# Performance work log

Hardware: AMD Instinct MI355X
Metric: run time of the kernel (lower is better)

Reference implementation:

```python
import jax, jax.numpy as jnp
import numpy as np

B, T, NCH, NBIN, NBAND = 2, 400, 8, 512, 40
NPV = NCH * NCH


def setup_inputs() -> dict:
    key = jax.random.key(0)
    ks = jax.random.split(key, 7)
    bins_real = jax.random.normal(ks[0], (B, T, NCH, NBIN), jnp.float32)
    bins_imag = jax.random.normal(ks[1], (B, T, NCH, NBIN), jnp.float32)
    band_matrix_real = jax.random.normal(ks[2], (NBIN, NBAND), jnp.float32) * 0.05
    band_matrix_imag = jax.random.normal(ks[3], (NBIN, NBAND), jnp.float32) * 0.05
    cov_to_pv_real = jax.random.normal(ks[4], (NPV, NCH * NCH), jnp.float32) * 0.1
    cov_to_pv_imag = jax.random.normal(ks[5], (NPV, NCH * NCH), jnp.float32) * 0.1
    tau = jax.random.uniform(ks[6], (NBAND,), jnp.float32, 0.8, 0.99)
    return {
        'bins_real': bins_real, 'bins_imag': bins_imag,
        'band_matrix_real': band_matrix_real, 'band_matrix_imag': band_matrix_imag,
        'cov_to_pv_real': cov_to_pv_real, 'cov_to_pv_imag': cov_to_pv_imag,
        'tau': tau,
    }


def _power_vector(bins_real, bins_imag, band_matrix_real, band_matrix_imag,
                  cov_to_pv_real, cov_to_pv_imag, tau):
    x = jax.lax.complex(bins_real, bins_imag)            # (B,T,C,F)
    nch = x.shape[-2]
    EPS = 1e-20
    # per-bin covariance outer product, flattened cov dim: (B,T,F,C*C)
    cov = jnp.einsum('btif,btjf->btfij', x, jnp.conj(x))
    b, t, f = cov.shape[:3]
    cov = cov.reshape(b, t, f, nch * nch)
    diag = jnp.arange(nch) * (nch + 1)                   # diagonal indices in cov dim
    trace = jnp.clip(jnp.sum(cov.real[..., diag], axis=-1, keepdims=True), EPS, None)
    cov = cov / trace                                    # per-bin trace normalisation
    # phase adjustment along the bin axis (n=1 -> lag of 2 bins)
    c = jnp.swapaxes(cov, -1, -2)                        # (B,T,C2,F)
    prod = jnp.conj(c[..., :-2]) * c[..., 2:]
    ang = jnp.arctan2(prod.imag, prod.real)
    ang = jnp.concatenate([ang[..., :1], ang, ang[..., -1:]], axis=-1)  # edge pad
    adj = jnp.abs(c) * jax.lax.complex(jnp.cos(ang), jnp.sin(ang))
    adj = adj.at[..., diag, :].set(c[..., diag, :])      # keep original diagonals
    # band projection: contract bins against (F,K) band matrix
    bm = jax.lax.complex(band_matrix_real, band_matrix_imag)
    band_cov = jnp.einsum('btcf,fk->btkc', adj, bm)      # (B,T,K,C2)
    dsum = jnp.clip(band_cov.real[..., diag].sum(-1, keepdims=True), EPS, None)
    band_cov = band_cov / dsum
    # first-order IIR smoothing over frames, per-band pole tau
    a = tau[:, None].astype(band_cov.real.dtype)         # (K,1)
    def step(carry, xt):
        y = a * carry + (1.0 - a) * xt
        return y, y
    y0 = jnp.zeros_like(band_cov[:, 0])                  # (B,K,C2)
    _, ys = jax.lax.scan(step, y0, jnp.moveaxis(band_cov, 1, 0))
    band_cov = jnp.moveaxis(ys, 0, 1)                    # (B,T,K,C2)
    # cov -> power vector projection, real part
    c2p = jax.lax.complex(cov_to_pv_real, cov_to_pv_imag)  # (P,C2)
    pv = jnp.einsum('pc,btkc->btkp', c2p, band_cov).real   # (B,T,K,P)
    return pv


def reference(bins_real, bins_imag, band_matrix_real, band_matrix_imag,
              cov_to_pv_real, cov_to_pv_imag, tau):
    return _power_vector(bins_real, bins_imag, band_matrix_real, band_matrix_imag,
                         cov_to_pv_real, cov_to_pv_imag, tau)
```

## Files before the change

kernel.cpp:

```cpp
#include <hip/hip_runtime.h>
#include <hip/hip_fp16.h>

#define B_    2
#define T_    400
#define NCH_  8
#define NBIN_ 512
#define NBAND_ 40
#define NPV_  64

using half8   = __attribute__((ext_vector_type(8))) _Float16;
using float4v = __attribute__((ext_vector_type(4))) float;

static __device__ inline unsigned pkhf(float x, float y) {
  __half2 h = __float22half2_rn(make_float2(x, y));
  return __builtin_bit_cast(unsigned, h);
}
static __device__ inline unsigned rot16(unsigned u) {
  return (u >> 16) | (u << 16);
}
static __device__ inline unsigned cmulc(unsigned viu, unsigned vju) {
  __half2 Vi = __builtin_bit_cast(__half2, viu);
  __half2 Vj = __builtin_bit_cast(__half2, vju);
  __half2 P1 = __hmul2(Vi, __low2half2(Vj));
  __half2 Qi = __lowhigh2highlow(Vi);
  unsigned tn = __builtin_bit_cast(unsigned, __high2half2(Vj)) ^ 0x80000000u;
  __half2 a  = __hfma2(Qi, __builtin_bit_cast(__half2, tn), P1);
  return __builtin_bit_cast(unsigned, a);
}

__global__ __launch_bounds__(256) void pv_prep(
    const float* __restrict__ bmr, const float* __restrict__ bmi,
    const float* __restrict__ c2pr, const float* __restrict__ c2pi,
    float* __restrict__ ws)
{
  const int tid = threadIdx.x;
  const int blk = blockIdx.x;
  if (blk == 0) {
    __shared__ float sds[256];
    int k = tid & 63, part = tid >> 6;
    float s = 0.f;
    if (k < NBAND_) {
      const float* col = bmr + k;
      #pragma unroll 16
      for (int f = part * 128; f < part * 128 + 128; f++) s += col[f * 40];
    }
    sds[tid] = s;
    __syncthreads();
    if (tid < NBAND_) {
      float t = sds[tid] + sds[tid + 64] + sds[tid + 128] + sds[tid + 192];
      ws[tid] = 1.0f / fmaxf(t, 1e-20f);
    }
  } else if (blk <= 24) {
    int F = (blk - 1) * 256 + tid;
    int l = F & 63;
    int fid = F >> 6;
    int s5 = fid / 3;
    int n = fid - s5 * 3;
    int k = n * 16 + (l & 15);
    int quad = l >> 4;
    unsigned dw[4];
    #pragma unroll
    for (int t2 = 0; t2 < 4; t2++) {
      float v0 = 0.f, v1 = 0.f;
      if (k < NBAND_) {
        int f = s5 * 16 + quad * 4 + t2;
        v0 = bmr[f * 40 + k]; v1 = bmi[f * 40 + k];
      }
      dw[t2] = pkhf(v0, v1);
    }
    ((uint4*)((char*)ws + 1024))[F] = make_uint4(dw[0], dw[1], dw[2], dw[3]);
  } else {
    int F2 = (blk - 25) * 256 + tid;
    int lane = F2 & 63, E = F2 >> 6;
    int nt = E >> 2, ks = E & 3;
    int n = lane & 15, quad = lane >> 4;
    int p = nt * 16 + n;
    unsigned dw[4];
    #pragma unroll
    for (int t2 = 0; t2 < 4; t2++) {
      int c = ks * 16 + quad * 4 + t2;
      dw[t2] = pkhf(c2pr[p * 64 + c], -c2pi[p * 64 + c]);
    }
    ((uint4*)((char*)ws + 197632))[E * 64 + lane] = make_uint4(dw[0], dw[1], dw[2], dw[3]);
  }
}

__global__ __launch_bounds__(256, 3) void pv_main(
    const float* __restrict__ br, const float* __restrict__ bi,
    const float* __restrict__ ws, float* __restrict__ out)
{
  __shared__ __align__(16) unsigned smem[12288];

  const int bt  = blockIdx.x;
  const int tid = threadIdx.x;

  const int mt   = tid >> 6;
  const int lane = tid & 63;
  const int m16  = lane & 15;
  const int quad = lane >> 4;
  const int p    = mt * 16 + m16;
  const int ich  = p >> 3, jch = p & 7;
  const uint4* BF0 = (const uint4*)((const char*)ws + 1024);
  unsigned* vsh = smem + 8192;

  {
    const float4* gr4 = (const float4*)(br + (size_t)bt * (NCH_ * NBIN_));
    const float4* gi4 = (const float4*)(bi + (size_t)bt * (NCH_ * NBIN_));
    float4* lr4 = (float4*)smem;
    float4* li4 = (float4*)(smem + 4096);
    #pragma unroll
    for (int it = 0; it < 4; it++) {
      lr4[it * 256 + tid] = gr4[it * 256 + tid];
      li4[it * 256 + tid] = gi4[it * 256 + tid];
    }
  }
  __syncthreads();

  {
    const float* rr = (const float*)smem;
    const float* ri = (const float*)(smem + 4096);
    #pragma unroll
    for (int fs = 0; fs < 2; fs++) {
      const int f = fs * 256 + tid;
      const int fm = (f == 0) ? 0 : ((f == 511) ? 509 : f - 1);
      const int fp = (f == 0) ? 2 : ((f == 511) ? 511 : f + 1);
      float tr = 0.f;
      float t1[8], t2[8];
      #pragma unroll
      for (int c = 0; c < 8; c++) {
        const float* cr = rr + c * 512;
        const float* ci = ri + c * 512;
        float xr = cr[f],   xi = ci[f];
        float xrm = cr[fm], xim = ci[fm];
        float xrp = cr[fp], xip = ci[fp];
        tr = fmaf(xr, xr, tr); tr = fmaf(xi, xi, tr);
        float Gr = fmaf(xrm, xrp,  xim * xip);
        float Gi = fmaf(xrm, xip, -(xim * xrp));
        float am = fmaxf(fmaxf(fabsf(Gr), fabsf(Gi)), 1e-30f);
        float rc = __builtin_amdgcn_rcpf(am);
        float q1 = Gr * rc, q2 = Gi * rc;
        float n2 = fmaf(q1, q1, q2 * q2);
        float rn = __builtin_amdgcn_rsqf(n2);
        bool ok = n2 > 0.f;
        float ur = ok ? q1 * rn : 1.f;
        float ui = ok ? q2 * rn : 0.f;
        float mg = __builtin_amdgcn_sqrtf(fmaf(xr, xr, xi * xi));
        t1[c] = mg * ur; t2[c] = mg * ui;
      }
      float scv = __builtin_amdgcn_rsqf(fmaxf(tr, 1e-20f));
      const int fc = f >> 2, fl = f & 3;
      #pragma unroll
      for (int c = 0; c < 8; c++)
        vsh[c * 512 + ((fc ^ c) << 2) + fl] = pkhf(t1[c] * scv, t2[c] * scv);
    }
  }
  __syncthreads();

  float4v acc[6];
  #pragma unroll
  for (int g = 0; g < 6; g++) acc[g] = (float4v){0.f, 0.f, 0.f, 0.f};

  const uint4* Bg = BF0 + lane;
  uint4 pa0 = Bg[0],   pa1 = Bg[64],  pa2 = Bg[128];
  uint4 pb0 = Bg[192], pb1 = Bg[256], pb2 = Bg[320];
  #pragma unroll 4
  for (int s = 0; s < 32; s++) {
    uint4 cb0 = pa0, cb1 = pa1, cb2 = pa2;
    pa0 = pb0; pa1 = pb1; pa2 = pb2;
    {
      const uint4* nx = Bg + (size_t)(((s + 2) & 31) * 192);
      pb0 = nx[0]; pb1 = nx[64]; pb2 = nx[128];
    }
    const int sc = s * 4 + quad;
    half8 b0 = __builtin_bit_cast(half8, cb0);
    half8 b1 = __builtin_bit_cast(half8, cb1);
    half8 b2 = __builtin_bit_cast(half8, cb2);
    const uint4* vb = (const uint4*)vsh;
    uint4 av = vb[ich * 128 + (sc ^ ich)];
    uint4 bv = vb[jch * 128 + (sc ^ jch)];
    unsigned a0 = cmulc(av.x, bv.x);
    unsigned a1 = cmulc(av.y, bv.y);
    unsigned a2 = cmulc(av.z, bv.z);
    unsigned a3 = cmulc(av.w, bv.w);
    uint4 au1 = make_uint4(a0 ^ 0x80000000u, a1 ^ 0x80000000u,
                           a2 ^ 0x80000000u, a3 ^ 0x80000000u);
    uint4 au2 = make_uint4(rot16(a0), rot16(a1),
                           rot16(a2), rot16(a3));
    half8 af1 = __builtin_bit_cast(half8, au1);
    half8 af2 = __builtin_bit_cast(half8, au2);
    acc[0] = __builtin_amdgcn_mfma_f32_16x16x32_f16(af1, b0, acc[0], 0, 0, 0);
    acc[3] = __builtin_amdgcn_mfma_f32_16x16x32_f16(af2, b0, acc[3], 0, 0, 0);
    acc[1] = __builtin_amdgcn_mfma_f32_16x16x32_f16(af1, b1, acc[1], 0, 0, 0);
    acc[4] = __builtin_amdgcn_mfma_f32_16x16x32_f16(af2, b1, acc[4], 0, 0, 0);
    acc[2] = __builtin_amdgcn_mfma_f32_16x16x32_f16(af1, b2, acc[2], 0, 0, 0);
    acc[5] = __builtin_amdgcn_mfma_f32_16x16x32_f16(af2, b2, acc[5], 0, 0, 0);
  }
  __syncthreads();

  const uint4* EF = ((const uint4*)((const char*)ws + 197632)) + (mt * 4) * 64 + lane;
  uint4 eb[4];
  #pragma unroll
  for (int ks = 0; ks < 4; ks++) eb[ks] = EF[ks * 64];

  {
    unsigned* bcsh = smem;
    #pragma unroll
    for (int n = 0; n < 3; n++) {
      uint4 w4 = make_uint4(pkhf(acc[n][0], acc[n+3][0]),
                            pkhf(acc[n][1], acc[n+3][1]),
                            pkhf(acc[n][2], acc[n+3][2]),
                            pkhf(acc[n][3], acc[n+3][3]));
      *(uint4*)(bcsh + (n * 16 + m16) * 68 + mt * 16 + quad * 4) = w4;
    }
  }
  __syncthreads();

  const float4* wsd = (const float4*)ws;
  {
    const unsigned* bcsh = smem;
    float4v eacc[3];
    #pragma unroll
    for (int kt = 0; kt < 3; kt++) eacc[kt] = (float4v){0.f, 0.f, 0.f, 0.f};
    #pragma unroll
    for (int ks = 0; ks < 4; ks++) {
      half8 bfr = __builtin_bit_cast(half8, eb[ks]);
      #pragma unroll
      for (int kt = 0; kt < 3; kt++) {
        uint4 a4 = *(const uint4*)(bcsh + (kt * 16 + m16) * 68 + ks * 16 + quad * 4);
        half8 afr = __builtin_bit_cast(half8, a4);
        eacc[kt] = __builtin_amdgcn_mfma_f32_16x16x32_f16(afr, bfr, eacc[kt], 0, 0, 0);
      }
    }
    float* op = out + (size_t)bt * (NBAND_ * NPV_);
    #pragma unroll
    for (int kt = 0; kt < 3; kt++) {
      float4 dv = wsd[kt * 4 + quad];
      float dva[4] = {dv.x, dv.y, dv.z, dv.w};
      #pragma unroll
      for (int r = 0; r < 4; r++) {
        int k = kt * 16 + quad * 4 + r;
        if (k < NBAND_)
          op[k * 64 + mt * 16 + m16] = eacc[kt][r] * dva[r];
      }
    }
  }
}

__global__ __launch_bounds__(512) void pv_iir4(float* __restrict__ z,
                                               const float* __restrict__ tau)
{
  __shared__ float gsh[16][32];
  const int ph = blockIdx.x & 1;
  const int bk = blockIdx.x >> 1;
  const int k = bk % NBAND_;
  const int b = bk / NBAND_;
  const float a  = tau[k];
  const float om = 1.0f - a;
  const int c  = threadIdx.x >> 5;
  const int pl = threadIdx.x & 31;
  const int p  = ph * 32 + pl;
  const size_t stride = (size_t)NBAND_ * 64;
  size_t idx0 = (size_t)b * (T_ * NBAND_ * 64) + (size_t)(c * 25) * stride + k * 64 + p;

  float y[25];
  float accv = 0.f;
  #pragma unroll
  for (int i = 0; i < 25; i++) {
    float v = z[idx0 + (size_t)i * stride];
    accv = fmaf(a, accv, om * v);
    y[i] = accv;
  }
  gsh[c][pl] = accv;
  __syncthreads();
  float a2 = a * a, a4 = a2 * a2, a8 = a4 * a4, a16 = a8 * a8;
  float A = a16 * a8 * a;
  float H = 0.f;
  #pragma unroll
  for (int d = 0; d < 15; d++) {
    float g = gsh[d][pl];
    H = (d < c) ? fmaf(A, H, g) : H;
  }
  float wp = a;
  #pragma unroll
  for (int i = 0; i < 25; i++) {
    z[idx0 + (size_t)i * stride] = fmaf(wp, H, y[i]);
    wp *= a;
  }
}

extern "C" void kernel_launch(void* const* d_in, const int* in_sizes, int n_in,
                              void* d_out, int out_size, void* d_ws, size_t ws_size,
                              hipStream_t stream)
{
  const float* br   = (const float*)d_in[0];
  const float* bi   = (const float*)d_in[1];
  const float* bmr  = (const float*)d_in[2];
  const float* bmi  = (const float*)d_in[3];
  const float* c2pr = (const float*)d_in[4];
  const float* c2pi = (const float*)d_in[5];
  const float* tau  = (const float*)d_in[6];
  float* out = (float*)d_out;
  float* ws  = (float*)d_ws;

  hipLaunchKernelGGL(pv_prep, dim3(29), dim3(256), 0, stream,
                     bmr, bmi, c2pr, c2pi, ws);
  hipLaunchKernelGGL(pv_main, dim3(B_ * T_), dim3(256), 0, stream,
                     br, bi, ws, out);
  hipLaunchKernelGGL(pv_iir4, dim3(B_ * NBAND_ * 2), dim3(512), 0, stream,
                     out, tau);
}
```

Measured before the change: 108.8 us.

## Stage band-matrix B fragments in LDS via async global_load_lds double buffering

```diff
diff --git a/kernel.cpp b/kernel.cpp
--- a/kernel.cpp
+++ b/kernel.cpp
@@ -26,6 +26,13 @@
   unsigned tn = __builtin_bit_cast(unsigned, __high2half2(Vj)) ^ 0x80000000u;
   __half2 a  = __hfma2(Qi, __builtin_bit_cast(__half2, tn), P1);
   return __builtin_bit_cast(unsigned, a);
+}
+static __device__ inline void gld_lds16(const uint4* g, uint4* l) {
+  auto* lds_ptr = reinterpret_cast<__attribute__((address_space(3))) uint4*>(
+      reinterpret_cast<uintptr_t>(l));
+  auto* g_ptr = reinterpret_cast<const __attribute__((address_space(1))) uint4*>(
+      reinterpret_cast<uintptr_t>(g));
+  __builtin_amdgcn_global_load_lds(g_ptr, lds_ptr, 16, 0, 0);
 }
 
 __global__ __launch_bounds__(256) void pv_prep(
@@ -156,46 +163,61 @@
   }
   __syncthreads();
 
+  uint4* bst = (uint4*)smem;
+  {
+    const uint4* g = BF0 + tid;
+    uint4* l = bst + tid;
+    gld_lds16(g, l);
+    gld_lds16(g + 256, l + 256);
+    gld_lds16(g + 512, l + 512);
+  }
+  __syncthreads();
+
   float4v acc[6];
   #pragma unroll
   for (int g = 0; g < 6; g++) acc[g] = (float4v){0.f, 0.f, 0.f, 0.f};
 
-  const uint4* Bg = BF0 + lane;
-  uint4 pa0 = Bg[0],   pa1 = Bg[64],  pa2 = Bg[128];
-  uint4 pb0 = Bg[192], pb1 = Bg[256], pb2 = Bg[320];
-  #pragma unroll 4
-  for (int s = 0; s < 32; s++) {
-    uint4 cb0 = pa0, cb1 = pa1, cb2 = pa2;
-    pa0 = pb0; pa1 = pb1; pa2 = pb2;
-    {
-      const uint4* nx = Bg + (size_t)(((s + 2) & 31) * 192);
-      pb0 = nx[0]; pb1 = nx[64]; pb2 = nx[128];
-    }
-    const int sc = s * 4 + quad;
-    half8 b0 = __builtin_bit_cast(half8, cb0);
-    half8 b1 = __builtin_bit_cast(half8, cb1);
-    half8 b2 = __builtin_bit_cast(half8, cb2);
-    const uint4* vb = (const uint4*)vsh;
-    uint4 av = vb[ich * 128 + (sc ^ ich)];
-    uint4 bv = vb[jch * 128 + (sc ^ jch)];
-    unsigned a0 = cmulc(av.x, bv.x);
-    unsigned a1 = cmulc(av.y, bv.y);
-    unsigned a2 = cmulc(av.z, bv.z);
-    unsigned a3 = cmulc(av.w, bv.w);
-    uint4 au1 = make_uint4(a0 ^ 0x80000000u, a1 ^ 0x80000000u,
-                           a2 ^ 0x80000000u, a3 ^ 0x80000000u);
-    uint4 au2 = make_uint4(rot16(a0), rot16(a1),
-                           rot16(a2), rot16(a3));
-    half8 af1 = __builtin_bit_cast(half8, au1);
-    half8 af2 = __builtin_bit_cast(half8, au2);
-    acc[0] = __builtin_amdgcn_mfma_f32_16x16x32_f16(af1, b0, acc[0], 0, 0, 0);
-    acc[3] = __builtin_amdgcn_mfma_f32_16x16x32_f16(af2, b0, acc[3], 0, 0, 0);
-    acc[1] = __builtin_amdgcn_mfma_f32_16x16x32_f16(af1, b1, acc[1], 0, 0, 0);
-    acc[4] = __builtin_amdgcn_mfma_f32_16x16x32_f16(af2, b1, acc[4], 0, 0, 0);
-    acc[2] = __builtin_amdgcn_mfma_f32_16x16x32_f16(af1, b2, acc[2], 0, 0, 0);
-    acc[5] = __builtin_amdgcn_mfma_f32_16x16x32_f16(af2, b2, acc[5], 0, 0, 0);
-  }
-  __syncthreads();
+  for (int st = 0; st < 8; st++) {
+    if (st < 7) {
+      const uint4* g = BF0 + (st + 1) * 768 + tid;
+      uint4* l = bst + ((st + 1) & 1) * 768 + tid;
+      gld_lds16(g, l);
+      gld_lds16(g + 256, l + 256);
+      gld_lds16(g + 512, l + 512);
+    }
+    const uint4* bb = bst + (st & 1) * 768;
+    #pragma unroll
+    for (int q = 0; q < 4; q++) {
+      const int s = st * 4 + q;
+      const int sc = s * 4 + quad;
+      uint4 cb0 = bb[(q * 3 + 0) * 64 + lane];
+      uint4 cb1 = bb[(q * 3 + 1) * 64 + lane];
+      uint4 cb2 = bb[(q * 3 + 2) * 64 + lane];
+      half8 b0 = __builtin_bit_cast(half8, cb0);
+      half8 b1 = __builtin_bit_cast(half8, cb1);
+      half8 b2 = __builtin_bit_cast(half8, cb2);
+      const uint4* vb = (const uint4*)vsh;
+      uint4 av = vb[ich * 128 + (sc ^ ich)];
+      uint4 bv = vb[jch * 128 + (sc ^ jch)];
+      unsigned a0 = cmulc(av.x, bv.x);
+      unsigned a1 = cmulc(av.y, bv.y);
+      unsigned a2 = cmulc(av.z, bv.z);
+      unsigned a3 = cmulc(av.w, bv.w);
+      uint4 au1 = make_uint4(a0 ^ 0x80000000u, a1 ^ 0x80000000u,
+                             a2 ^ 0x80000000u, a3 ^ 0x80000000u);
+      uint4 au2 = make_uint4(rot16(a0), rot16(a1),
+                             rot16(a2), rot16(a3));
+      half8 af1 = __builtin_bit_cast(half8, au1);
+      half8 af2 = __builtin_bit_cast(half8, au2);
+      acc[0] = __builtin_amdgcn_mfma_f32_16x16x32_f16(af1, b0, acc[0], 0, 0, 0);
+      acc[3] = __builtin_amdgcn_mfma_f32_16x16x32_f16(af2, b0, acc[3], 0, 0, 0);
+      acc[1] = __builtin_amdgcn_mfma_f32_16x16x32_f16(af1, b1, acc[1], 0, 0, 0);
+      acc[4] = __builtin_amdgcn_mfma_f32_16x16x32_f16(af2, b1, acc[4], 0, 0, 0);
+      acc[2] = __builtin_amdgcn_mfma_f32_16x16x32_f16(af1, b2, acc[2], 0, 0, 0);
+      acc[5] = __builtin_amdgcn_mfma_f32_16x16x32_f16(af2, b2, acc[5], 0, 0, 0);
+    }
+    __syncthreads();
+  }
 
   const uint4* EF = ((const uint4*)((const char*)ws + 197632)) + (mt * 4) * 64 + lane;
   uint4 eb[4];
```

New measurement: 112.9 us. 3.7% more time.
